# Kernel optimization log

Measured on AMD Instinct MI355X. Metric: run time of the kernel, lower is better.

## Reference

```python
import jax, jax.numpy as jnp
import numpy as np

B, NUM_GENES, F = 8, 20000, 128
N, E, H = 50000, 800000, 128


def setup_inputs() -> dict:
    key = jax.random.key(0)
    k = jax.random.split(key, 8)
    gene_emb = jax.random.normal(k[0], (B, NUM_GENES, F), dtype=jnp.float32)
    W1 = jax.random.normal(k[1], (F, H), dtype=jnp.float32) * 0.05
    b1 = jnp.zeros((H,), dtype=jnp.float32)
    W2 = jax.random.normal(k[2], (H, H), dtype=jnp.float32) * 0.05
    b2 = jnp.zeros((H,), dtype=jnp.float32)
    global_ids = jax.random.randint(k[3], (N,), 0, NUM_GENES, dtype=jnp.int64)
    edge_index = jax.random.randint(k[4], (2, E), 0, N, dtype=jnp.int64)
    return {"gene_emb": gene_emb, "W1": W1, "b1": b1, "W2": W2, "b2": b2,
            "global_ids": global_ids, "edge_index": edge_index}


def reference(gene_emb, W1, b1, W2, b2, global_ids, edge_index):
    n = global_ids.shape[0]
    # GCN normalization with self-loops (PyG GCNConv default):
    # A_hat = A + I, deg over target nodes, norm = d^{-1/2}[src] * d^{-1/2}[dst]
    loop = jnp.arange(n)
    src = jnp.concatenate([edge_index[0], loop])  # [E+N]
    dst = jnp.concatenate([edge_index[1], loop])  # [E+N]
    deg = jnp.zeros((n,), gene_emb.dtype).at[dst].add(1.0)
    dinv = jax.lax.rsqrt(deg)  # deg >= 1 thanks to self-loops
    norm = (dinv[src] * dinv[dst])[None, :, None]  # [1, E+N, 1]

    def gcn(x, W, b):
        h = x @ W                                   # [B, N, H] transform first (linear commutes)
        msg = h[:, src, :] * norm                   # gather + scale: [B, E+N, H]
        agg = jnp.zeros_like(h).at[:, dst].add(msg)  # scatter-add over targets
        return agg + b

    x = gene_emb[:, global_ids, :]                  # [B, N, F] node feature gather
    x = jax.nn.relu(gcn(x, W1, b1))
    x = gcn(x, W2, b2)
    # global_mean_pool: each batch replica is one whole graph -> mean over nodes
    return x.mean(axis=1)                           # [B, H]
```

## Files before the change

kernel.cpp:

```cpp
#include <hip/hip_runtime.h>

#define NG 20000
#define BB 8
#define FD 128
#define H1 1250

typedef unsigned int uint;
typedef unsigned short ushort;
typedef __attribute__((ext_vector_type(8))) short short8v;
typedef __attribute__((ext_vector_type(4))) float float4v;
typedef __attribute__((ext_vector_type(4))) int int4v;
typedef __attribute__((ext_vector_type(2))) float f2v;

__device__ f2v llvm_rbl_v2f32(int4v srsrc, int voffset, int soffset, int aux)
    __asm("llvm.amdgcn.raw.buffer.load.v2f32");

__device__ __forceinline__ int4v make_srsrc(const void* p) {
    int4v r;
    r.x = (int)(uint)(uintptr_t)p;
    r.y = (int)(uint)((uintptr_t)p >> 32);
    r.z = -1;
    r.w = 0x00020000;
    return r;
}

__device__ __forceinline__ ushort f2bf(float x) {
    uint u = __float_as_uint(x);
    u += 0x7FFFu + ((u >> 16) & 1u);
    return (ushort)(u >> 16);
}
__device__ __forceinline__ float bf_lo(uint u) { return __uint_as_float(u << 16); }
__device__ __forceinline__ float bf_hi(uint u) { return __uint_as_float(u & 0xFFFF0000u); }

__device__ __forceinline__ void h_tile(char* smem, int hb,
                                       const float* __restrict__ gene,
                                       const ushort* __restrict__ w1t,
                                       uint* __restrict__ h2u, int t) {
    ushort* Al = (ushort*)smem;
    ushort* Bl = (ushort*)(smem + 16384);
    float*  Cl = (float*)smem;
    int p  = hb & 3;
    int g0 = (hb >> 2) * 32;

#pragma unroll
    for (int s = 0; s < 8; s++) {
        int f = t + s * 256;
        int r = f >> 5, k0 = (f & 31) * 4;
        int bb = 2 * p + (r >> 5);
        int gg = g0 + (r & 31);
        float4 v = *(const float4*)(gene + ((size_t)bb * NG + gg) * 128 + k0);
        ushort4 u;
        u.x = f2bf(v.x); u.y = f2bf(v.y); u.z = f2bf(v.z); u.w = f2bf(v.w);
        int byte = (r * 256 + k0 * 2) ^ ((r & 7) << 4);
        *(ushort4*)(smem + byte) = u;
    }
#pragma unroll
    for (int s = 0; s < 8; s++) {
        int f = t + s * 256;
        int j = f >> 4, k0 = (f & 15) * 8;
        uint4 v = *(const uint4*)(w1t + j * 128 + k0);
        int byte = (j * 256 + k0 * 2) ^ ((j & 7) << 4);
        *(uint4*)((char*)Bl + byte) = v;
    }
    __syncthreads();

    int wid = t >> 6, lane = t & 63;
    int r0 = wid * 16;
    int lrow = lane & 15, lhi = lane >> 4;
    float4v acc[8];
#pragma unroll
    for (int nf = 0; nf < 8; nf++) acc[nf] = (float4v)(0.f);

#pragma unroll
    for (int c = 0; c < 4; c++) {
        int ra = r0 + lrow;
        int byteA = (ra * 256 + (c * 32 + lhi * 8) * 2) ^ ((ra & 7) << 4);
        short8v a = *(short8v*)((char*)Al + byteA);
#pragma unroll
        for (int nf = 0; nf < 8; nf++) {
            int jb = nf * 16 + lrow;
            int byteB = (jb * 256 + (c * 32 + lhi * 8) * 2) ^ ((jb & 7) << 4);
            short8v b = *(short8v*)((char*)Bl + byteB);
            acc[nf] = __builtin_amdgcn_mfma_f32_16x16x32_bf16(a, b, acc[nf], 0, 0, 0);
        }
    }
    __syncthreads();

#pragma unroll
    for (int nf = 0; nf < 8; nf++) {
#pragma unroll
        for (int q = 0; q < 4; q++) {
            Cl[(r0 + lhi * 4 + q) * 128 + nf * 16 + lrow] = acc[nf][q];
        }
    }
    __syncthreads();

#pragma unroll
    for (int s = 0; s < 16; s++) {
        int flat = t + s * 256;
        int gi = flat >> 7, cc = flat & 127;
        float lo = Cl[gi * 128 + cc];
        float hi = Cl[(32 + gi) * 128 + cc];
        uint u = (uint)f2bf(lo) | ((uint)f2bf(hi) << 16);
        h2u[((size_t)p * NG + g0 + gi) * 128 + cc] = u;
    }
}

__global__ void k_setup(int* ideg, float* s_acc, int* ticket,
                        const float* __restrict__ W1, ushort* w1t, int N) {
    int i = blockIdx.x * blockDim.x + threadIdx.x;
    if (i < N) ideg[i] = 0;
    if (i < 8 * BB * FD) s_acc[i] = 0.0f;
    if (i == 0) *ticket = 0;
    if (i < FD * FD) {
        int j = i >> 7, k = i & 127;
        w1t[i] = f2bf(W1[k * 128 + j]);
    }
}

__global__ __launch_bounds__(256, 3)
void k_counth(const int* __restrict__ dst, int* ideg, int E, int eb,
              const float* __restrict__ gene, const ushort* __restrict__ w1t,
              uint* __restrict__ h2u) {
    __shared__ __align__(16) char smem[49152];
    if ((int)blockIdx.x < eb) {
        int e = blockIdx.x * 256 + threadIdx.x;
        if (e < E) atomicAdd(&ideg[dst[e]], 1);
        return;
    }
    h_tile(smem, blockIdx.x - eb, gene, w1t, h2u, threadIdx.x);
}

__global__ void k_scan(const int* __restrict__ ideg, float* dinv, float* cval,
                       int* padcnt, int* offs, const int* __restrict__ gid,
                       int* cursor, int2* csr, int* ticket, int N) {
    __shared__ int sd[256];
    __shared__ int sbase;
    int t = threadIdx.x, idx = blockIdx.x * 256 + t;
    int v = 0, d = 0;
    float iv = 0.f;
    if (idx < N) {
        d = ideg[idx] + 1;
        float fd = (float)d;
        dinv[idx] = rsqrtf(fd);
        iv = 1.0f / fd;
        cval[idx] = iv;
        v = (d + 7) & ~7;
        padcnt[idx] = v;
    }
    sd[t] = v; __syncthreads();
    for (int o = 1; o < 256; o <<= 1) {
        int x = (t >= o) ? sd[t - o] : 0;
        __syncthreads();
        sd[t] += x;
        __syncthreads();
    }
    if (t == 255) sbase = atomicAdd(ticket, sd[255]);
    __syncthreads();
    if (idx < N) {
        int o = sbase + sd[t] - v;
        offs[idx] = o;
        csr[o] = make_int2(gid[idx], __float_as_int(iv));
        cursor[idx] = 1;
        for (int z = d; z < v; z++) csr[o + z] = make_int2(0, 0);
    }
}

__global__ __launch_bounds__(256, 3)
void k_fillh(const int* __restrict__ src, const int* __restrict__ dst,
             const int* __restrict__ gid, const float* __restrict__ dinv,
             float* cval, const int* __restrict__ offs, int* cursor,
             int2* csr, int E, int eb,
             const float* __restrict__ gene, const ushort* __restrict__ w1t,
             uint* __restrict__ h2u) {
    __shared__ __align__(16) char smem[49152];
    if ((int)blockIdx.x < eb) {
        int e = blockIdx.x * 256 + threadIdx.x;
        if (e >= E) return;
        int s = src[e], d = dst[e];
        float nrm = dinv[s] * dinv[d];
        atomicAdd(&cval[s], nrm);
        int pos = atomicAdd(&cursor[d], 1);
        csr[offs[d] + pos] = make_int2(gid[s], __float_as_int(nrm));
        return;
    }
    h_tile(smem, (int)blockIdx.x - eb + H1, gene, w1t, h2u, threadIdx.x);
}

__global__ __launch_bounds__(512)
void k_aggp(const uint* __restrict__ hp, const int2* __restrict__ csr,
            const int* __restrict__ offs, const int* __restrict__ padcnt,
            const float* __restrict__ cval, const float* __restrict__ b1,
            float* __restrict__ s_acc, int N, int wpp) {
    int p    = blockIdx.x & 3;
    int wid  = threadIdx.x >> 6, lane = threadIdx.x & 63;
    int w    = __builtin_amdgcn_readfirstlane((blockIdx.x >> 2) * 8 + wid);
    int4v sr = make_srsrc(hp + (size_t)p * NG * 128);
    int voff = lane * 8;
    int l2 = lane * 2;
    float bx = b1[l2], by = b1[l2 + 1];
    float sx0 = 0.f, sx1 = 0.f, sy0 = 0.f, sy1 = 0.f;

    int i0 = (int)((long long)w * N / wpp);
    int i1 = (int)((long long)(w + 1) * N / wpp);
    for (int i = i0; i < i1; ++i) {
        int   e  = offs[i];
        int   pc = padcnt[i];
        float cv = cval[i];
        float ax0 = 0.f, ax1 = 0.f, ay0 = 0.f, ay1 = 0.f;
        for (int q = 0; q < pc; q += 8) {
            int ee = e + q;
            int2 c0 = csr[ee],     c1 = csr[ee + 1], c2 = csr[ee + 2], c3 = csr[ee + 3];
            int2 c4 = csr[ee + 4], c5 = csr[ee + 5], c6 = csr[ee + 6], c7 = csr[ee + 7];
            f2v u0 = llvm_rbl_v2f32(sr, voff, c0.x << 9, 0);
            f2v u1 = llvm_rbl_v2f32(sr, voff, c1.x << 9, 0);
            f2v u2 = llvm_rbl_v2f32(sr, voff, c2.x << 9, 0);
            f2v u3 = llvm_rbl_v2f32(sr, voff, c3.x << 9, 0);
            f2v u4 = llvm_rbl_v2f32(sr, voff, c4.x << 9, 0);
            f2v u5 = llvm_rbl_v2f32(sr, voff, c5.x << 9, 0);
            f2v u6 = llvm_rbl_v2f32(sr, voff, c6.x << 9, 0);
            f2v u7 = llvm_rbl_v2f32(sr, voff, c7.x << 9, 0);
            float n0 = __int_as_float(c0.y), n1 = __int_as_float(c1.y);
            float n2 = __int_as_float(c2.y), n3 = __int_as_float(c3.y);
            float n4 = __int_as_float(c4.y), n5 = __int_as_float(c5.y);
            float n6 = __int_as_float(c6.y), n7 = __int_as_float(c7.y);
            uint a, b;
            a = __float_as_uint(u0.x); b = __float_as_uint(u0.y);
            ax0 = fmaf(n0, bf_lo(a), ax0); ax1 = fmaf(n0, bf_hi(a), ax1);
            ay0 = fmaf(n0, bf_lo(b), ay0); ay1 = fmaf(n0, bf_hi(b), ay1);
            a = __float_as_uint(u1.x); b = __float_as_uint(u1.y);
            ax0 = fmaf(n1, bf_lo(a), ax0); ax1 = fmaf(n1, bf_hi(a), ax1);
            ay0 = fmaf(n1, bf_lo(b), ay0); ay1 = fmaf(n1, bf_hi(b), ay1);
            a = __float_as_uint(u2.x); b = __float_as_uint(u2.y);
            ax0 = fmaf(n2, bf_lo(a), ax0); ax1 = fmaf(n2, bf_hi(a), ax1);
            ay0 = fmaf(n2, bf_lo(b), ay0); ay1 = fmaf(n2, bf_hi(b), ay1);
            a = __float_as_uint(u3.x); b = __float_as_uint(u3.y);
            ax0 = fmaf(n3, bf_lo(a), ax0); ax1 = fmaf(n3, bf_hi(a), ax1);
            ay0 = fmaf(n3, bf_lo(b), ay0); ay1 = fmaf(n3, bf_hi(b), ay1);
            a = __float_as_uint(u4.x); b = __float_as_uint(u4.y);
            ax0 = fmaf(n4, bf_lo(a), ax0); ax1 = fmaf(n4, bf_hi(a), ax1);
            ay0 = fmaf(n4, bf_lo(b), ay0); ay1 = fmaf(n4, bf_hi(b), ay1);
            a = __float_as_uint(u5.x); b = __float_as_uint(u5.y);
            ax0 = fmaf(n5, bf_lo(a), ax0); ax1 = fmaf(n5, bf_hi(a), ax1);
            ay0 = fmaf(n5, bf_lo(b), ay0); ay1 = fmaf(n5, bf_hi(b), ay1);
            a = __float_as_uint(u6.x); b = __float_as_uint(u6.y);
            ax0 = fmaf(n6, bf_lo(a), ax0); ax1 = fmaf(n6, bf_hi(a), ax1);
            ay0 = fmaf(n6, bf_lo(b), ay0); ay1 = fmaf(n6, bf_hi(b), ay1);
            a = __float_as_uint(u7.x); b = __float_as_uint(u7.y);
            ax0 = fmaf(n7, bf_lo(a), ax0); ax1 = fmaf(n7, bf_hi(a), ax1);
            ay0 = fmaf(n7, bf_lo(b), ay0); ay1 = fmaf(n7, bf_hi(b), ay1);
        }
        sx0 += cv * fmaxf(ax0 + bx, 0.f);
        sx1 += cv * fmaxf(ax1 + bx, 0.f);
        sy0 += cv * fmaxf(ay0 + by, 0.f);
        sy1 += cv * fmaxf(ay1 + by, 0.f);
    }

    __shared__ float red[8][256];
    red[wid][lane * 4 + 0] = sx0;
    red[wid][lane * 4 + 1] = sx1;
    red[wid][lane * 4 + 2] = sy0;
    red[wid][lane * 4 + 3] = sy1;
    __syncthreads();
    int t = threadIdx.x;
    if (t < 256) {
        float s = 0.f;
#pragma unroll
        for (int wv = 0; wv < 8; wv++) s += red[wv][t];
        int l = t >> 2, c = t & 3;
        int rep = (blockIdx.x >> 2) & 7;
        atomicAdd(&s_acc[rep * 1024 + (2 * p + (c & 1)) * 128 + 2 * l + (c >> 1)], s);
    }
}

__global__ void k_final(const float* __restrict__ s_acc, const float* __restrict__ W2,
                        const float* __restrict__ b2, float* __restrict__ out, float invN) {
    __shared__ float ss[1024];
    int t = threadIdx.x;
    for (int idx = t; idx < 1024; idx += 128) {
        float s = 0.f;
#pragma unroll
        for (int r = 0; r < 8; r++) s += s_acc[r * 1024 + idx];
        ss[idx] = s;
    }
    __syncthreads();
    float acc[8];
#pragma unroll
    for (int b = 0; b < 8; b++) acc[b] = 0.f;
    for (int k = 0; k < 128; k++) {
        float w = W2[k * 128 + t];
#pragma unroll
        for (int b = 0; b < 8; b++) acc[b] += ss[b * 128 + k] * w;
    }
    float bb = b2[t];
#pragma unroll
    for (int b = 0; b < 8; b++) out[b * 128 + t] = acc[b] * invN + bb;
}


extern "C" void kernel_launch(void* const* d_in, const int* in_sizes, int n_in,
                              void* d_out, int out_size, void* d_ws, size_t ws_size,
                              hipStream_t stream) {
    const float* gene = (const float*)d_in[0];
    const float* W1   = (const float*)d_in[1];
    const float* b1   = (const float*)d_in[2];
    const float* W2   = (const float*)d_in[3];
    const float* b2   = (const float*)d_in[4];
    const int*   gid  = (const int*)d_in[5];
    const int*   eidx = (const int*)d_in[6];
    int N = in_sizes[5];
    int E = in_sizes[6] / 2;
    const int* src = eidx;
    const int* dst = eidx + E;
    float* out = (float*)d_out;

    char* p = (char*)d_ws;
    auto alloc = [&](size_t bytes) -> char* {
        char* r = p; p += (bytes + 255) & ~(size_t)255; return r;
    };
    size_t csr_cap = (size_t)E + 8 * (size_t)N;
    int*   ideg   = (int*)  alloc((size_t)N * 4);
    float* dinv   = (float*)alloc((size_t)N * 4);
    float* cval   = (float*)alloc((size_t)N * 4);
    int*   padcnt = (int*)  alloc((size_t)N * 4);
    int*   offs   = (int*)  alloc((size_t)N * 4);
    int*   cursor = (int*)  alloc((size_t)N * 4);
    int*   ticket = (int*)  alloc(256);
    int2*  csr    = (int2*) alloc(csr_cap * 8);
    float* s_acc  = (float*)alloc(8 * 1024 * 4);
    uint*  h2     = (uint*) alloc((size_t)NG * BB * FD * 2);
    ushort* w1t   = (ushort*)alloc(128 * 128 * 2);

    int nb = (N + 255) / 256;
    int eb = (E + 255) / 256;
    int hblk = 4 * (NG / 32);

    const int NBLK = 2048;
    int wpp = (NBLK / 4) * 8;

    k_setup <<<nb, 256, 0, stream>>>(ideg, s_acc, ticket, W1, w1t, N);
    k_counth<<<eb + H1, 256, 0, stream>>>(dst, ideg, E, eb, gene, w1t, h2);
    k_scan  <<<nb, 256, 0, stream>>>(ideg, dinv, cval, padcnt, offs, gid,
                                     cursor, csr, ticket, N);
    k_fillh <<<eb + (hblk - H1), 256, 0, stream>>>(src, dst, gid, dinv, cval, offs,
                                                   cursor, csr, E, eb, gene, w1t, h2);
    k_aggp  <<<NBLK, 512, 0, stream>>>(h2, csr, offs, padcnt,
                                       cval, b1, s_acc, N, wpp);
    k_final <<<1, 128, 0, stream>>>(s_acc, W2, b2, out, 1.0f / (float)N);
}
```

Measured before the change: 305.9 us.

## Record edge slot during degree count and overlap scan with H tiles

The degree-count pass now stores the value returned by its atomic increment for each edge, so the fill pass can compute the CSR slot directly instead of doing a second atomic on a cursor array. The scan kernel also takes part of the dense transform tiles, spreading them over three launches so the small scan kernel overlaps with GEMM work. The cost is an extra E-sized int array that is written and then read back.

```diff
diff --git a/kernel.cpp b/kernel.cpp
--- a/kernel.cpp
+++ b/kernel.cpp
@@ -3,7 +3,8 @@
 #define NG 20000
 #define BB 8
 #define FD 128
-#define H1 1250
+#define HA 1000
+#define HB 300
 
 typedef unsigned int uint;
 typedef unsigned short ushort;
@@ -119,22 +120,30 @@
 }
 
 __global__ __launch_bounds__(256, 3)
-void k_counth(const int* __restrict__ dst, int* ideg, int E, int eb,
+void k_counth(const int* __restrict__ dst, int* ideg, int* epos, int E, int eb,
               const float* __restrict__ gene, const ushort* __restrict__ w1t,
               uint* __restrict__ h2u) {
     __shared__ __align__(16) char smem[49152];
     if ((int)blockIdx.x < eb) {
         int e = blockIdx.x * 256 + threadIdx.x;
-        if (e < E) atomicAdd(&ideg[dst[e]], 1);
+        if (e < E) epos[e] = atomicAdd(&ideg[dst[e]], 1);
         return;
     }
     h_tile(smem, blockIdx.x - eb, gene, w1t, h2u, threadIdx.x);
 }
 
-__global__ void k_scan(const int* __restrict__ ideg, float* dinv, float* cval,
-                       int* padcnt, int* offs, const int* __restrict__ gid,
-                       int* cursor, int2* csr, int* ticket, int N) {
-    __shared__ int sd[256];
+__global__ __launch_bounds__(256, 3)
+void k_scanh(const int* __restrict__ ideg, float* dinv, float* cval,
+             int* padcnt, int* offs, const int* __restrict__ gid,
+             int2* csr, int* ticket, int N, int nb,
+             const float* __restrict__ gene, const ushort* __restrict__ w1t,
+             uint* __restrict__ h2u) {
+    __shared__ __align__(16) char smem[49152];
+    if ((int)blockIdx.x >= nb) {
+        h_tile(smem, (int)blockIdx.x - nb + HA, gene, w1t, h2u, threadIdx.x);
+        return;
+    }
+    int* sd = (int*)smem;
     __shared__ int sbase;
     int t = threadIdx.x, idx = blockIdx.x * 256 + t;
     int v = 0, d = 0;
@@ -161,7 +170,6 @@
         int o = sbase + sd[t] - v;
         offs[idx] = o;
         csr[o] = make_int2(gid[idx], __float_as_int(iv));
-        cursor[idx] = 1;
         for (int z = d; z < v; z++) csr[o + z] = make_int2(0, 0);
     }
 }
@@ -169,7 +177,8 @@
 __global__ __launch_bounds__(256, 3)
 void k_fillh(const int* __restrict__ src, const int* __restrict__ dst,
              const int* __restrict__ gid, const float* __restrict__ dinv,
-             float* cval, const int* __restrict__ offs, int* cursor,
+             float* cval, const int* __restrict__ offs,
+             const int* __restrict__ epos,
              int2* csr, int E, int eb,
              const float* __restrict__ gene, const ushort* __restrict__ w1t,
              uint* __restrict__ h2u) {
@@ -180,11 +189,10 @@
         int s = src[e], d = dst[e];
         float nrm = dinv[s] * dinv[d];
         atomicAdd(&cval[s], nrm);
-        int pos = atomicAdd(&cursor[d], 1);
-        csr[offs[d] + pos] = make_int2(gid[s], __float_as_int(nrm));
+        csr[offs[d] + 1 + epos[e]] = make_int2(gid[s], __float_as_int(nrm));
         return;
     }
-    h_tile(smem, (int)blockIdx.x - eb + H1, gene, w1t, h2u, threadIdx.x);
+    h_tile(smem, (int)blockIdx.x - eb + HA + HB, gene, w1t, h2u, threadIdx.x);
 }
 
 __global__ __launch_bounds__(512)
@@ -324,7 +332,7 @@
     float* cval   = (float*)alloc((size_t)N * 4);
     int*   padcnt = (int*)  alloc((size_t)N * 4);
     int*   offs   = (int*)  alloc((size_t)N * 4);
-    int*   cursor = (int*)  alloc((size_t)N * 4);
+    int*   epos   = (int*)  alloc((size_t)E * 4);
     int*   ticket = (int*)  alloc(256);
     int2*  csr    = (int2*) alloc(csr_cap * 8);
     float* s_acc  = (float*)alloc(8 * 1024 * 4);
@@ -339,11 +347,11 @@
     int wpp = (NBLK / 4) * 8;
 
     k_setup <<<nb, 256, 0, stream>>>(ideg, s_acc, ticket, W1, w1t, N);
-    k_counth<<<eb + H1, 256, 0, stream>>>(dst, ideg, E, eb, gene, w1t, h2);
-    k_scan  <<<nb, 256, 0, stream>>>(ideg, dinv, cval, padcnt, offs, gid,
-                                     cursor, csr, ticket, N);
-    k_fillh <<<eb + (hblk - H1), 256, 0, stream>>>(src, dst, gid, dinv, cval, offs,
-                                                   cursor, csr, E, eb, gene, w1t, h2);
+    k_counth<<<eb + HA, 256, 0, stream>>>(dst, ideg, epos, E, eb, gene, w1t, h2);
+    k_scanh <<<nb + HB, 256, 0, stream>>>(ideg, dinv, cval, padcnt, offs, gid,
+                                          csr, ticket, N, nb, gene, w1t, h2);
+    k_fillh <<<eb + (hblk - HA - HB), 256, 0, stream>>>(src, dst, gid, dinv, cval, offs,
+                                                        epos, csr, E, eb, gene, w1t, h2);
     k_aggp  <<<NBLK, 512, 0, stream>>>(h2, csr, offs, padcnt,
                                        cval, b1, s_acc, N, wpp);
     k_final <<<1, 128, 0, stream>>>(s_acc, W2, b2, out, 1.0f / (float)N);
```

Result: faster. 275.2 us, median of 2 (-10.0%).
